# Kernel tuning notes

Measured on AMD Instinct MI355X. Metric: run time of the kernel, lower is better.

The kernel has to match this reference:

```python
import jax, jax.numpy as jnp
import numpy as np
import math

B, CIN, COUT, K, SD, H, W = 16, 512, 512, 3, 512, 32, 32


def setup_inputs() -> dict:
    key = jax.random.key(0)
    ks = jax.random.split(key, 7)
    return {
        "x": jax.random.normal(ks[0], (B, CIN, H, W), jnp.float32),
        "style": jax.random.normal(ks[1], (B, SD), jnp.float32),
        "noise": jax.random.normal(ks[2], (B, 1, H, W), jnp.float32),
        "weight": jax.random.normal(ks[3], (COUT, CIN, K, K), jnp.float32),
        "mod_w": jax.random.normal(ks[4], (CIN, SD), jnp.float32),
        "mod_b": jnp.ones((CIN,), jnp.float32),
        "noise_weight": jax.random.normal(ks[5], (1,), jnp.float32) * 0.1,
        "act_bias": jax.random.normal(ks[6], (COUT,), jnp.float32) * 0.1,
    }


def reference(x, style, noise, weight, mod_w, mod_b, noise_weight, act_bias):
    conv_scale = 1.0 / math.sqrt(CIN * K * K)  # equalized-lr scale of ModulatedConv2d
    mod_scale = 1.0 / math.sqrt(SD)            # EqualLinear scale (lr_mul=1)

    # style modulation: EqualLinear(style_dim -> in_channel), bias init 1
    s = style @ (mod_w.T * mod_scale) + mod_b              # [B, CIN]

    # per-sample modulated weights [B, COUT, CIN, K, K]
    w = conv_scale * weight[None] * s[:, None, :, None, None]

    # demodulation
    demod = jax.lax.rsqrt(jnp.sum(w * w, axis=(2, 3, 4)) + 1e-8)  # [B, COUT]
    w = w * demod[:, :, None, None, None]

    # grouped (per-sample) conv: vmap a single-sample conv over the batch
    pad = K // 2

    def conv1(xi, wi):
        return jax.lax.conv_general_dilated(
            xi[None], wi, window_strides=(1, 1),
            padding=[(pad, pad), (pad, pad)],
            dimension_numbers=("NCHW", "OIHW", "NCHW"))[0]

    out = jax.vmap(conv1)(x, w)  # [B, COUT, H, W]

    # NoiseInjection: out + weight * noise (scalar learned weight)
    out = out + noise_weight[0] * noise

    # FusedLeakyReLU: leaky_relu(out + bias, 0.2) * sqrt(2)
    out = jax.nn.leaky_relu(out + act_bias[None, :, None, None], 0.2) * math.sqrt(2.0)
    return out
```

## Files before the change

kernel.cpp:

```cpp
#include <hip/hip_runtime.h>
#include <cstdint>
#include <cstddef>

typedef unsigned short u16;
typedef __attribute__((ext_vector_type(8))) short short8;
typedef __attribute__((ext_vector_type(4))) float f32x4;

#define CIN   512
#define COUT  512
#define BATCH 16
#define HWSZ  1024
#define PADW  34

static constexpr float MOD_SCALE  = 0.044194173824159216f;
static constexpr float CONV_SCALE = 0.014731391274719739f;

#define WS_S    0
#define WS_DSC  (32*1024)
#define WS_WSQ  (64*1024)
#define WS_WBT  (64*1024 + 1024*1024)
#define WS_XSP  (WS_WBT + 9*512*512*2)

__device__ __forceinline__ u16 f2bf(float f) {
  union { float f; uint32_t u; } v; v.f = f;
  uint32_t r = v.u + 0x7fffu + ((v.u >> 16) & 1u);
  return (u16)(r >> 16);
}

__device__ __forceinline__ void gload16(const void* g, void* l) {
  __builtin_amdgcn_global_load_lds(
      (const __attribute__((address_space(1))) void*)g,
      (__attribute__((address_space(3))) void*)l, 16, 0, 0);
}

__global__ void k_style(const float* __restrict__ style, const float* __restrict__ mod_w,
                        const float* __restrict__ mod_b, float* __restrict__ s_out) {
  int gid  = blockIdx.x * blockDim.x + threadIdx.x;
  int w    = gid >> 6, lane = gid & 63;
  int b    = w >> 9, i = w & 511;
  const float4* st = (const float4*)(style + (size_t)b * 512);
  const float4* mw = (const float4*)(mod_w + (size_t)i * 512);
  float4 a0 = st[lane * 2], a1 = st[lane * 2 + 1];
  float4 w0 = mw[lane * 2], w1 = mw[lane * 2 + 1];
  float acc = a0.x*w0.x + a0.y*w0.y + a0.z*w0.z + a0.w*w0.w
            + a1.x*w1.x + a1.y*w1.y + a1.z*w1.z + a1.w*w1.w;
  #pragma unroll
  for (int off = 32; off; off >>= 1) acc += __shfl_xor(acc, off);
  if (lane == 0) s_out[w] = acc * MOD_SCALE + mod_b[i];
}

__global__ void k_wprep(const float* __restrict__ w, float* __restrict__ wsq,
                        u16* __restrict__ wbt2) {
  int idx = blockIdx.x * 256 + threadIdx.x;
  int o = idx >> 9, i = idx & 511;
  const float* p = w + (size_t)idx * 9;
  float a = 0.f;
  #pragma unroll
  for (int kxy = 0; kxy < 9; ++kxy) {
    float v = p[kxy];
    a += v * v;
    wbt2[((size_t)(kxy * 64 + (i >> 3)) * 512 + o) * 8 + (i & 7)] = f2bf(v);
  }
  wsq[idx] = a;
}

__global__ void k_dscale(const float* __restrict__ wsq, const float* __restrict__ s,
                         float* __restrict__ dsc) {
  int gid  = blockIdx.x * blockDim.x + threadIdx.x;
  int w    = gid >> 6, lane = gid & 63;
  int b    = w >> 9, o = w & 511;
  const float4* q4 = (const float4*)(wsq + (size_t)o * 512);
  const float4* s4 = (const float4*)(s   + (size_t)b * 512);
  float4 q0 = q4[lane * 2], q1 = q4[lane * 2 + 1];
  float4 t0 = s4[lane * 2], t1 = s4[lane * 2 + 1];
  float acc = q0.x*t0.x*t0.x + q0.y*t0.y*t0.y + q0.z*t0.z*t0.z + q0.w*t0.w*t0.w
            + q1.x*t1.x*t1.x + q1.y*t1.y*t1.y + q1.z*t1.z*t1.z + q1.w*t1.w*t1.w;
  #pragma unroll
  for (int off = 32; off; off >>= 1) acc += __shfl_xor(acc, off);
  if (lane == 0)
    dsc[w] = CONV_SCALE * rsqrtf(acc * CONV_SCALE * CONV_SCALE + 1e-8f);
}

__global__ void k_halo(u16* __restrict__ xsp) {
  int cell = blockIdx.x;
  int b = blockIdx.y;
  int y, x;
  if (cell < 34)       { y = 0;          x = cell; }
  else if (cell < 68)  { y = 33;         x = cell - 34; }
  else if (cell < 100) { y = cell - 67;  x = 0; }
  else                 { y = cell - 99;  x = 33; }
  uint32_t* p = (uint32_t*)(xsp + ((size_t)(b * PADW + y) * PADW + x) * 512);
  p[threadIdx.x] = 0;
}

__global__ void k_xs(const float* __restrict__ x, const float* __restrict__ s,
                     u16* __restrict__ xsp) {
  __shared__ float tile[64][33];
  int icb = blockIdx.x, y = blockIdx.y, b = blockIdx.z;
  int t = threadIdx.x;
  int i0 = icb * 64;
  int c  = t & 31;
  int r0 = t >> 5;
  #pragma unroll
  for (int it = 0; it < 8; ++it) {
    int row = r0 + it * 8;
    float sv = s[b * 512 + i0 + row];
    tile[row][c] = x[((size_t)(b * 512 + i0 + row)) * 1024 + y * 32 + c] * sv;
  }
  __syncthreads();
  int il = t & 63;
  int x0 = t >> 6;
  #pragma unroll
  for (int it = 0; it < 8; ++it) {
    int xc = x0 + it * 4;
    xsp[((size_t)((b * PADW + y + 1) * PADW) + (xc + 1)) * 512 + i0 + il] = f2bf(tile[il][xc]);
  }
}

__global__ __launch_bounds__(512, 2) void k_conv(
    const u16* __restrict__ wbt2, const u16* __restrict__ xsp,
    const float* __restrict__ dsc, const float* __restrict__ noise,
    const float* __restrict__ nw, const float* __restrict__ abias,
    float* __restrict__ out)
{
  __shared__ u16 Bld[3 * 8192];

  const int tid  = threadIdx.x;
  const int wave = tid >> 6, lane = tid & 63;

  const int bid = blockIdx.x;
  const int swz = (bid & 7) * 32 + (bid >> 3);
  const int o0 = (swz >> 7) << 8;
  const int m0 = (swz & 127) << 7;
  const int b  = m0 >> 10;

  const int wo = (wave >> 1) * 64;
  const int wm = (wave & 1) * 64;
  const int lrow = lane & 15;
  const int lk   = (lane >> 4) * 8;
  const int rsw  = (lrow & 7) << 3;

  const u16* pA = wbt2 + (size_t)(lane >> 4) * 4096 + (size_t)(o0 + wo + lrow) * 8;

  const int cc = (((lane & 7) ^ (lane >> 3)) * 8);
  const u16* gB[2]; int lBo[2];
  #pragma unroll
  for (int q = 0; q < 2; ++q) {
    int r = wave * 16 + q * 8 + (lane >> 3);
    int mg = m0 + r;
    int yy = (mg >> 5) & 31, xx = mg & 31;
    gB[q] = xsp + ((size_t)(b * PADW + yy) * PADW + xx) * 512 + cc;
    lBo[q] = (wave * 16 + q * 8) * 64;
  }

  f32x4 acc[4][4];
  #pragma unroll
  for (int i = 0; i < 4; ++i)
    #pragma unroll
    for (int j = 0; j < 4; ++j) acc[i][j] = (f32x4){0.f, 0.f, 0.f, 0.f};

  short8 av0[2][4], av1[2][4];

  auto avload = [&](int ks, short8 (&dst)[2][4]) {
    const u16* base = pA + (size_t)(ks >> 3) * 262144 + (size_t)(ks & 7) * 32768;
    #pragma unroll
    for (int kh = 0; kh < 2; ++kh)
      #pragma unroll
      for (int mi = 0; mi < 4; ++mi)
        dst[kh][mi] = *(const short8*)(base + kh * 16384 + mi * 128);
  };

  auto stageB = [&](int ks, int bufi) {
    int kxy = ks >> 3, ib = (ks & 7) << 6;
    int ky = kxy / 3, kx = kxy - ky * 3;
    int offB = ((ky * PADW + kx) << 9) + ib;
    int sb = bufi * 8192;
    #pragma unroll
    for (int q = 0; q < 2; ++q) gload16(gB[q] + offB, &Bld[sb + lBo[q]]);
  };

  auto compute = [&](const short8 (&av)[2][4], int bufi) {
    const int cb = bufi * 8192;
    __builtin_amdgcn_s_setprio(1);
    #pragma unroll
    for (int kh = 0; kh < 2; ++kh) {
      int kos = (kh * 32 + lk) ^ rsw;
      short8 bv[4];
      #pragma unroll
      for (int ni = 0; ni < 4; ++ni)
        bv[ni] = *(const short8*)&Bld[cb + (wm + ni * 16 + lrow) * 64 + kos];
      #pragma unroll
      for (int mi = 0; mi < 4; ++mi)
        #pragma unroll
        for (int ni = 0; ni < 4; ++ni)
          acc[mi][ni] = __builtin_amdgcn_mfma_f32_16x16x32_bf16(
              av[kh][mi], bv[ni], acc[mi][ni], 0, 0, 0);
    }
    __builtin_amdgcn_s_setprio(0);
  };

  stageB(0, 0);
  stageB(1, 1);
  avload(0, av0);

#define STEP(KS, AVCUR, AVNXT, BBUF, BNXT, DOAV, DOSTAGE, WN)            \
  {                                                                      \
    if (DOAV) avload((KS) + 1, AVNXT);                                   \
    __builtin_amdgcn_sched_barrier(0);                                   \
    asm volatile("s_waitcnt vmcnt(" #WN ")" ::: "memory");               \
    __builtin_amdgcn_s_barrier();                                        \
    __builtin_amdgcn_sched_barrier(0);                                   \
    if (DOSTAGE) stageB((KS) + 2, BNXT);                                 \
    compute(AVCUR, BBUF);                                                \
  }

  for (int t = 0; t < 11; ++t) {
    const int k0 = t * 6;
    STEP(k0 + 0, av0, av1, 0, 2, 1, 1, 8);
    STEP(k0 + 1, av1, av0, 1, 0, 1, 1, 8);
    STEP(k0 + 2, av0, av1, 2, 1, 1, 1, 8);
    STEP(k0 + 3, av1, av0, 0, 2, 1, 1, 8);
    STEP(k0 + 4, av0, av1, 1, 0, 1, 1, 8);
    STEP(k0 + 5, av1, av0, 2, 1, 1, 1, 8);
  }
  STEP(66, av0, av1, 0, 2, 1, 1, 8);
  STEP(67, av1, av0, 1, 0, 1, 1, 8);
  STEP(68, av0, av1, 2, 1, 1, 1, 8);
  STEP(69, av1, av0, 0, 2, 1, 1, 8);
  STEP(70, av0, av1, 1, 0, 1, 0, 8);
  STEP(71, av1, av0, 2, 1, 0, 0, 0);
#undef STEP

  const float nwv = nw[0];
  const int mrow = (lane >> 4) << 2;
  #pragma unroll
  for (int mi = 0; mi < 4; ++mi) {
    #pragma unroll
    for (int ni = 0; ni < 4; ++ni) {
      int mg = m0 + wm + ni * 16 + lrow;
      int hw = mg & 1023;
      float nz = nwv * noise[b * 1024 + hw];
      #pragma unroll
      for (int r = 0; r < 4; ++r) {
        int og = o0 + wo + mi * 16 + mrow + r;
        float v = acc[mi][ni][r] * dsc[b * 512 + og] + nz + abias[og];
        v = (v > 0.f ? v : 0.2f * v) * 1.4142135623730951f;
        out[(size_t)(b * 512 + og) * 1024 + hw] = v;
      }
    }
  }
}

extern "C" void kernel_launch(void* const* d_in, const int* in_sizes, int n_in,
                              void* d_out, int out_size, void* d_ws, size_t ws_size,
                              hipStream_t stream) {
  const float* x      = (const float*)d_in[0];
  const float* style  = (const float*)d_in[1];
  const float* noise  = (const float*)d_in[2];
  const float* weight = (const float*)d_in[3];
  const float* mod_w  = (const float*)d_in[4];
  const float* mod_b  = (const float*)d_in[5];
  const float* nw     = (const float*)d_in[6];
  const float* abias  = (const float*)d_in[7];
  float* out = (float*)d_out;

  char* ws = (char*)d_ws;
  float* s_buf = (float*)(ws + WS_S);
  float* dsc   = (float*)(ws + WS_DSC);
  float* wsq   = (float*)(ws + WS_WSQ);
  u16*   wbt2  = (u16*)(ws + WS_WBT);
  u16*   xsp   = (u16*)(ws + WS_XSP);

  k_halo  <<<dim3(132, 16), 256, 0, stream>>>(xsp);
  k_style <<<2048, 256, 0, stream>>>(style, mod_w, mod_b, s_buf);
  k_wprep <<<1024, 256, 0, stream>>>(weight, wsq, wbt2);
  k_dscale<<<2048, 256, 0, stream>>>(wsq, s_buf, dsc);
  k_xs    <<<dim3(8, 32, 16), 256, 0, stream>>>(x, s_buf, xsp);
  k_conv  <<<256, 512, 0, stream>>>(wbt2, xsp, dsc, noise, nw, abias, out);
}
```

Measured before the change: 105.2 us.

## Deepen conv B-tile pipeline to four LDS stages with register-prefetched fragments

```diff
diff --git a/kernel.cpp b/kernel.cpp
--- a/kernel.cpp
+++ b/kernel.cpp
@@ -123,7 +123,7 @@
     const float* __restrict__ nw, const float* __restrict__ abias,
     float* __restrict__ out)
 {
-  __shared__ u16 Bld[3 * 8192];
+  __shared__ u16 Bld[4 * 8192];
 
   const int tid  = threadIdx.x;
   const int wave = tid >> 6, lane = tid & 63;
@@ -160,6 +160,7 @@
     for (int j = 0; j < 4; ++j) acc[i][j] = (f32x4){0.f, 0.f, 0.f, 0.f};
 
   short8 av0[2][4], av1[2][4];
+  short8 bv0[2][4], bv1[2][4];
 
   auto avload = [&](int ks, short8 (&dst)[2][4]) {
     const u16* base = pA + (size_t)(ks >> 3) * 262144 + (size_t)(ks & 7) * 32768;
@@ -179,56 +180,61 @@
     for (int q = 0; q < 2; ++q) gload16(gB[q] + offB, &Bld[sb + lBo[q]]);
   };
 
-  auto compute = [&](const short8 (&av)[2][4], int bufi) {
+  auto bvread = [&](int bufi, short8 (&dst)[2][4]) {
     const int cb = bufi * 8192;
-    __builtin_amdgcn_s_setprio(1);
     #pragma unroll
     for (int kh = 0; kh < 2; ++kh) {
       int kos = (kh * 32 + lk) ^ rsw;
-      short8 bv[4];
       #pragma unroll
       for (int ni = 0; ni < 4; ++ni)
-        bv[ni] = *(const short8*)&Bld[cb + (wm + ni * 16 + lrow) * 64 + kos];
+        dst[kh][ni] = *(const short8*)&Bld[cb + (wm + ni * 16 + lrow) * 64 + kos];
+    }
+  };
+
+  auto compute = [&](const short8 (&av)[2][4], const short8 (&bv)[2][4]) {
+    __builtin_amdgcn_s_setprio(1);
+    #pragma unroll
+    for (int kh = 0; kh < 2; ++kh)
       #pragma unroll
       for (int mi = 0; mi < 4; ++mi)
         #pragma unroll
         for (int ni = 0; ni < 4; ++ni)
           acc[mi][ni] = __builtin_amdgcn_mfma_f32_16x16x32_bf16(
-              av[kh][mi], bv[ni], acc[mi][ni], 0, 0, 0);
-    }
+              av[kh][mi], bv[kh][ni], acc[mi][ni], 0, 0, 0);
     __builtin_amdgcn_s_setprio(0);
   };
 
   stageB(0, 0);
   stageB(1, 1);
+  stageB(2, 2);
   avload(0, av0);
-
-#define STEP(KS, AVCUR, AVNXT, BBUF, BNXT, DOAV, DOSTAGE, WN)            \
+  asm volatile("s_waitcnt vmcnt(12)" ::: "memory");
+  __builtin_amdgcn_s_barrier();
+  __builtin_amdgcn_sched_barrier(0);
+  bvread(0, bv0);
+
+#define STEP(KS, BSTG, BRD, AVC, AVN, BVC, BVN, DOSTG, DOAV, DOBV)       \
   {                                                                      \
-    if (DOAV) avload((KS) + 1, AVNXT);                                   \
-    __builtin_amdgcn_sched_barrier(0);                                   \
-    asm volatile("s_waitcnt vmcnt(" #WN ")" ::: "memory");               \
+    asm volatile("s_waitcnt vmcnt(10)" ::: "memory");                    \
     __builtin_amdgcn_s_barrier();                                        \
     __builtin_amdgcn_sched_barrier(0);                                   \
-    if (DOSTAGE) stageB((KS) + 2, BNXT);                                 \
-    compute(AVCUR, BBUF);                                                \
-  }
-
-  for (int t = 0; t < 11; ++t) {
-    const int k0 = t * 6;
-    STEP(k0 + 0, av0, av1, 0, 2, 1, 1, 8);
-    STEP(k0 + 1, av1, av0, 1, 0, 1, 1, 8);
-    STEP(k0 + 2, av0, av1, 2, 1, 1, 1, 8);
-    STEP(k0 + 3, av1, av0, 0, 2, 1, 1, 8);
-    STEP(k0 + 4, av0, av1, 1, 0, 1, 1, 8);
-    STEP(k0 + 5, av1, av0, 2, 1, 1, 1, 8);
-  }
-  STEP(66, av0, av1, 0, 2, 1, 1, 8);
-  STEP(67, av1, av0, 1, 0, 1, 1, 8);
-  STEP(68, av0, av1, 2, 1, 1, 1, 8);
-  STEP(69, av1, av0, 0, 2, 1, 1, 8);
-  STEP(70, av0, av1, 1, 0, 1, 0, 8);
-  STEP(71, av1, av0, 2, 1, 0, 0, 0);
+    if (DOSTG) stageB((KS) + 3, BSTG);                                   \
+    if (DOAV)  avload((KS) + 1, AVN);                                    \
+    if (DOBV)  bvread(BRD, BVN);                                         \
+    compute(AVC, BVC);                                                   \
+  }
+
+  for (int t = 0; t < 17; ++t) {
+    const int k0 = t * 4;
+    STEP(k0 + 0, 3, 1, av0, av1, bv0, bv1, 1, 1, 1);
+    STEP(k0 + 1, 0, 2, av1, av0, bv1, bv0, 1, 1, 1);
+    STEP(k0 + 2, 1, 3, av0, av1, bv0, bv1, 1, 1, 1);
+    STEP(k0 + 3, 2, 0, av1, av0, bv1, bv0, 1, 1, 1);
+  }
+  STEP(68, 3, 1, av0, av1, bv0, bv1, 1, 1, 1);
+  STEP(69, 0, 2, av1, av0, bv1, bv0, 0, 1, 1);
+  STEP(70, 1, 3, av0, av1, bv0, bv1, 0, 1, 1);
+  STEP(71, 2, 0, av1, av0, bv1, bv0, 0, 0, 0);
 #undef STEP
 
   const float nwv = nw[0];
```

New measurement: 109.4 us. 4.0% more time.

## Restructure conv GEMM to per-wave private LDS pipelines with larger warp tiles

Applied to the files above, without the earlier changes.

```diff
diff --git a/kernel.cpp b/kernel.cpp
--- a/kernel.cpp
+++ b/kernel.cpp
@@ -117,13 +117,13 @@
   }
 }
 
-__global__ __launch_bounds__(512, 2) void k_conv(
+__global__ __launch_bounds__(256, 1) void k_conv(
     const u16* __restrict__ wbt2, const u16* __restrict__ xsp,
     const float* __restrict__ dsc, const float* __restrict__ noise,
     const float* __restrict__ nw, const float* __restrict__ abias,
     float* __restrict__ out)
 {
-  __shared__ u16 Bld[3 * 8192];
+  extern __shared__ u16 SM[];
 
   const int tid  = threadIdx.x;
   const int wave = tid >> 6, lane = tid & 63;
@@ -134,107 +134,108 @@
   const int m0 = (swz & 127) << 7;
   const int b  = m0 >> 10;
 
-  const int wo = (wave >> 1) * 64;
-  const int wm = (wave & 1) * 64;
+  const int wo = (wave >> 1) << 7;
+  const int wm = (wave & 1) << 6;
   const int lrow = lane & 15;
-  const int lk   = (lane >> 4) * 8;
-  const int rsw  = (lrow & 7) << 3;
-
-  const u16* pA = wbt2 + (size_t)(lane >> 4) * 4096 + (size_t)(o0 + wo + lrow) * 8;
-
-  const int cc = (((lane & 7) ^ (lane >> 3)) * 8);
-  const u16* gB[2]; int lBo[2];
-  #pragma unroll
-  for (int q = 0; q < 2; ++q) {
-    int r = wave * 16 + q * 8 + (lane >> 3);
-    int mg = m0 + r;
+  const int kc   = lane >> 4;
+
+  u16* Abuf = &SM[wave * 18432];
+  u16* Bbuf = &SM[wave * 18432 + 12288];
+
+  const u16* gA = wbt2 + ((size_t)(o0 + wo) + lane) * 8;
+
+  const u16* gB[4];
+  #pragma unroll
+  for (int r = 0; r < 4; ++r) {
+    int row = r * 16 + (lane >> 2);
+    int ck  = (lane & 3) ^ ((row & 3) ^ ((row >> 2) & 3));
+    int mg  = m0 + wm + row;
     int yy = (mg >> 5) & 31, xx = mg & 31;
-    gB[q] = xsp + ((size_t)(b * PADW + yy) * PADW + xx) * 512 + cc;
-    lBo[q] = (wave * 16 + q * 8) * 64;
-  }
-
-  f32x4 acc[4][4];
-  #pragma unroll
-  for (int i = 0; i < 4; ++i)
+    gB[r] = xsp + ((size_t)(b * PADW + yy) * PADW + xx) * 512 + ck * 8;
+  }
+
+  f32x4 acc[8][4];
+  #pragma unroll
+  for (int i = 0; i < 8; ++i)
     #pragma unroll
     for (int j = 0; j < 4; ++j) acc[i][j] = (f32x4){0.f, 0.f, 0.f, 0.f};
 
-  short8 av0[2][4], av1[2][4];
-
-  auto avload = [&](int ks, short8 (&dst)[2][4]) {
-    const u16* base = pA + (size_t)(ks >> 3) * 262144 + (size_t)(ks & 7) * 32768;
-    #pragma unroll
-    for (int kh = 0; kh < 2; ++kh)
-      #pragma unroll
-      for (int mi = 0; mi < 4; ++mi)
-        dst[kh][mi] = *(const short8*)(base + kh * 16384 + mi * 128);
+  short8 av0[8], av1[8], bv0[4], bv1[4];
+
+  auto stage = [&](int ks, int s) {
+    const u16* as = gA + (size_t)(4 * ks) * 4096;
+    u16* ad = Abuf + s * 4096;
+    #pragma unroll
+    for (int r = 0; r < 8; ++r)
+      gload16(as + (r >> 1) * 4096 + (r & 1) * 512,
+              ad + (r >> 1) * 1024 + (r & 1) * 512);
+    int kxy = ks >> 4;
+    int ky = kxy / 3, kx = kxy - ky * 3;
+    int offB = ((ky * PADW + kx) << 9) + (ks & 15) * 32;
+    u16* bd = Bbuf + s * 2048;
+    #pragma unroll
+    for (int r = 0; r < 4; ++r)
+      gload16(gB[r] + offB, bd + r * 512);
   };
 
-  auto stageB = [&](int ks, int bufi) {
-    int kxy = ks >> 3, ib = (ks & 7) << 6;
-    int ky = kxy / 3, kx = kxy - ky * 3;
-    int offB = ((ky * PADW + kx) << 9) + ib;
-    int sb = bufi * 8192;
-    #pragma unroll
-    for (int q = 0; q < 2; ++q) gload16(gB[q] + offB, &Bld[sb + lBo[q]]);
-  };
-
-  auto compute = [&](const short8 (&av)[2][4], int bufi) {
-    const int cb = bufi * 8192;
-    __builtin_amdgcn_s_setprio(1);
-    #pragma unroll
-    for (int kh = 0; kh < 2; ++kh) {
-      int kos = (kh * 32 + lk) ^ rsw;
-      short8 bv[4];
-      #pragma unroll
-      for (int ni = 0; ni < 4; ++ni)
-        bv[ni] = *(const short8*)&Bld[cb + (wm + ni * 16 + lrow) * 64 + kos];
-      #pragma unroll
-      for (int mi = 0; mi < 4; ++mi)
-        #pragma unroll
-        for (int ni = 0; ni < 4; ++ni)
-          acc[mi][ni] = __builtin_amdgcn_mfma_f32_16x16x32_bf16(
-              av[kh][mi], bv[ni], acc[mi][ni], 0, 0, 0);
-    }
-    __builtin_amdgcn_s_setprio(0);
-  };
-
-  stageB(0, 0);
-  stageB(1, 1);
-  avload(0, av0);
-
-#define STEP(KS, AVCUR, AVNXT, BBUF, BNXT, DOAV, DOSTAGE, WN)            \
+#define RD(S, AV, BV)                                                     \
+  {                                                                       \
+    const u16* pa = Abuf + (S) * 4096 + kc * 1024 + lrow * 8;             \
+    _Pragma("unroll")                                                     \
+    for (int mi = 0; mi < 8; ++mi)                                        \
+      AV[mi] = *(const short8*)(pa + mi * 128);                           \
+    _Pragma("unroll")                                                     \
+    for (int ni = 0; ni < 4; ++ni) {                                      \
+      int row = ni * 16 + lrow;                                           \
+      int ckr = kc ^ ((row & 3) ^ ((row >> 2) & 3));                      \
+      BV[ni] = *(const short8*)(Bbuf + (S) * 2048 + row * 32 + ckr * 8);  \
+    }                                                                     \
+  }
+
+#define COMPUTE(AV, BV)                                                   \
+  _Pragma("unroll")                                                       \
+  for (int mi = 0; mi < 8; ++mi)                                          \
+    _Pragma("unroll")                                                     \
+    for (int ni = 0; ni < 4; ++ni)                                        \
+      acc[mi][ni] = __builtin_amdgcn_mfma_f32_16x16x32_bf16(              \
+          AV[mi], BV[ni], acc[mi][ni], 0, 0, 0);
+
+  stage(0, 0);
+  stage(1, 1);
+  asm volatile("s_waitcnt vmcnt(12)" ::: "memory");
+  RD(0, av0, bv0);
+
+#define STEP(KS, SNX, SRD, AVN, BVN, AVC, BVC, DOSTG, DORD, VM)          \
   {                                                                      \
-    if (DOAV) avload((KS) + 1, AVNXT);                                   \
-    __builtin_amdgcn_sched_barrier(0);                                   \
-    asm volatile("s_waitcnt vmcnt(" #WN ")" ::: "memory");               \
-    __builtin_amdgcn_s_barrier();                                        \
-    __builtin_amdgcn_sched_barrier(0);                                   \
-    if (DOSTAGE) stageB((KS) + 2, BNXT);                                 \
-    compute(AVCUR, BBUF);                                                \
-  }
-
-  for (int t = 0; t < 11; ++t) {
+    if (DOSTG) stage((KS) + 2, SNX);                                     \
+    asm volatile("s_waitcnt vmcnt(" #VM ")" ::: "memory");               \
+    if (DORD) RD(SRD, AVN, BVN);                                         \
+    COMPUTE(AVC, BVC);                                                   \
+  }
+
+  for (int t = 0; t < 23; ++t) {
     const int k0 = t * 6;
-    STEP(k0 + 0, av0, av1, 0, 2, 1, 1, 8);
-    STEP(k0 + 1, av1, av0, 1, 0, 1, 1, 8);
-    STEP(k0 + 2, av0, av1, 2, 1, 1, 1, 8);
-    STEP(k0 + 3, av1, av0, 0, 2, 1, 1, 8);
-    STEP(k0 + 4, av0, av1, 1, 0, 1, 1, 8);
-    STEP(k0 + 5, av1, av0, 2, 1, 1, 1, 8);
-  }
-  STEP(66, av0, av1, 0, 2, 1, 1, 8);
-  STEP(67, av1, av0, 1, 0, 1, 1, 8);
-  STEP(68, av0, av1, 2, 1, 1, 1, 8);
-  STEP(69, av1, av0, 0, 2, 1, 1, 8);
-  STEP(70, av0, av1, 1, 0, 1, 0, 8);
-  STEP(71, av1, av0, 2, 1, 0, 0, 0);
+    STEP(k0 + 0, 2, 1, av1, bv1, av0, bv0, 1, 1, 12);
+    STEP(k0 + 1, 0, 2, av0, bv0, av1, bv1, 1, 1, 12);
+    STEP(k0 + 2, 1, 0, av1, bv1, av0, bv0, 1, 1, 12);
+    STEP(k0 + 3, 2, 1, av0, bv0, av1, bv1, 1, 1, 12);
+    STEP(k0 + 4, 0, 2, av1, bv1, av0, bv0, 1, 1, 12);
+    STEP(k0 + 5, 1, 0, av0, bv0, av1, bv1, 1, 1, 12);
+  }
+  STEP(138, 2, 1, av1, bv1, av0, bv0, 1, 1, 12);
+  STEP(139, 0, 2, av0, bv0, av1, bv1, 1, 1, 12);
+  STEP(140, 1, 0, av1, bv1, av0, bv0, 1, 1, 12);
+  STEP(141, 2, 1, av0, bv0, av1, bv1, 1, 1, 12);
+  STEP(142, 0, 2, av1, bv1, av0, bv0, 0, 1, 0);
+  STEP(143, 0, 0, av0, bv0, av1, bv1, 0, 0, 0);
 #undef STEP
+#undef RD
+#undef COMPUTE
 
   const float nwv = nw[0];
   const int mrow = (lane >> 4) << 2;
   #pragma unroll
-  for (int mi = 0; mi < 4; ++mi) {
+  for (int mi = 0; mi < 8; ++mi) {
     #pragma unroll
     for (int ni = 0; ni < 4; ++ni) {
       int mg = m0 + wm + ni * 16 + lrow;
@@ -271,10 +272,13 @@
   u16*   wbt2  = (u16*)(ws + WS_WBT);
   u16*   xsp   = (u16*)(ws + WS_XSP);
 
+  hipFuncSetAttribute((const void*)k_conv,
+                      hipFuncAttributeMaxDynamicSharedMemorySize, 147456);
+
   k_halo  <<<dim3(132, 16), 256, 0, stream>>>(xsp);
   k_style <<<2048, 256, 0, stream>>>(style, mod_w, mod_b, s_buf);
   k_wprep <<<1024, 256, 0, stream>>>(weight, wsq, wbt2);
   k_dscale<<<2048, 256, 0, stream>>>(wsq, s_buf, dsc);
   k_xs    <<<dim3(8, 32, 16), 256, 0, stream>>>(x, s_buf, xsp);
-  k_conv  <<<256, 512, 0, stream>>>(wbt2, xsp, dsc, noise, nw, abias, out);
-}
+  k_conv  <<<256, 256, 147456, stream>>>(wbt2, xsp, dsc, noise, nw, abias, out);
+}
```

New measurement: 116.0 us. +10.3%, slower.

## Stage input halo tile once per channel chunk and reuse across all 3x3 taps

Applied to the files above, without the earlier changes.

```diff
diff --git a/kernel.cpp b/kernel.cpp
--- a/kernel.cpp
+++ b/kernel.cpp
@@ -25,12 +25,6 @@
   union { float f; uint32_t u; } v; v.f = f;
   uint32_t r = v.u + 0x7fffu + ((v.u >> 16) & 1u);
   return (u16)(r >> 16);
-}
-
-__device__ __forceinline__ void gload16(const void* g, void* l) {
-  __builtin_amdgcn_global_load_lds(
-      (const __attribute__((address_space(1))) void*)g,
-      (__attribute__((address_space(3))) void*)l, 16, 0, 0);
 }
 
 __global__ void k_style(const float* __restrict__ style, const float* __restrict__ mod_w,
@@ -117,13 +111,13 @@
   }
 }
 
-__global__ __launch_bounds__(512, 2) void k_conv(
+__global__ __launch_bounds__(512, 1) void k_conv(
     const u16* __restrict__ wbt2, const u16* __restrict__ xsp,
     const float* __restrict__ dsc, const float* __restrict__ noise,
     const float* __restrict__ nw, const float* __restrict__ abias,
     float* __restrict__ out)
 {
-  __shared__ u16 Bld[3 * 8192];
+  __shared__ u16 H[2][13824];
 
   const int tid  = threadIdx.x;
   const int wave = tid >> 6, lane = tid & 63;
@@ -133,24 +127,42 @@
   const int o0 = (swz >> 7) << 8;
   const int m0 = (swz & 127) << 7;
   const int b  = m0 >> 10;
+  const int y0 = (m0 & 1023) >> 5;
 
   const int wo = (wave >> 1) * 64;
   const int wm = (wave & 1) * 64;
   const int lrow = lane & 15;
-  const int lk   = (lane >> 4) * 8;
-  const int rsw  = (lrow & 7) << 3;
-
-  const u16* pA = wbt2 + (size_t)(lane >> 4) * 4096 + (size_t)(o0 + wo + lrow) * 8;
-
-  const int cc = (((lane & 7) ^ (lane >> 3)) * 8);
-  const u16* gB[2]; int lBo[2];
-  #pragma unroll
-  for (int q = 0; q < 2; ++q) {
-    int r = wave * 16 + q * 8 + (lane >> 3);
-    int mg = m0 + r;
-    int yy = (mg >> 5) & 31, xx = mg & 31;
-    gB[q] = xsp + ((size_t)(b * PADW + yy) * PADW + xx) * 512 + cc;
-    lBo[q] = (wave * 16 + q * 8) * 64;
+  const int g    = lane >> 4;
+
+  const u16* pA = wbt2 + (size_t)g * 4096 + (size_t)(o0 + wo + lrow) * 8;
+
+  int offs[4][3][2];
+  #pragma unroll
+  for (int ni = 0; ni < 4; ++ni) {
+    int mloc = wm + ni * 16 + lrow;
+    int yb = mloc >> 5, xb = mloc & 31;
+    #pragma unroll
+    for (int kx = 0; kx < 3; ++kx) {
+      int xx = xb + kx;
+      #pragma unroll
+      for (int kh = 0; kh < 2; ++kh) {
+        int c = (kh * 4 + g) ^ (xx & 7);
+        offs[ni][kx][kh] = (((yb * 36 + xx) * 64) + c * 8) * 2;
+      }
+    }
+  }
+
+  int hsrc[4], hdst[4];
+  bool hval[4];
+  #pragma unroll
+  for (int r = 0; r < 4; ++r) {
+    int T = r * 512 + wave * 64 + lane;
+    hval[r] = (T < 1632);
+    int Tc = hval[r] ? T : 0;
+    int yy = Tc / 272, rem = Tc % 272;
+    int xx = rem >> 3, c = rem & 7;
+    hsrc[r] = ((b * 34 + y0 + yy) * 34 + xx) * 512 + c * 8;
+    hdst[r] = (yy * 36 + xx) * 64 + ((c ^ (xx & 7)) * 8);
   }
 
   f32x4 acc[4][4];
@@ -160,76 +172,91 @@
     for (int j = 0; j < 4; ++j) acc[i][j] = (f32x4){0.f, 0.f, 0.f, 0.f};
 
   short8 av0[2][4], av1[2][4];
-
-  auto avload = [&](int ks, short8 (&dst)[2][4]) {
-    const u16* base = pA + (size_t)(ks >> 3) * 262144 + (size_t)(ks & 7) * 32768;
-    #pragma unroll
-    for (int kh = 0; kh < 2; ++kh)
-      #pragma unroll
-      for (int mi = 0; mi < 4; ++mi)
-        dst[kh][mi] = *(const short8*)(base + kh * 16384 + mi * 128);
-  };
-
-  auto stageB = [&](int ks, int bufi) {
-    int kxy = ks >> 3, ib = (ks & 7) << 6;
-    int ky = kxy / 3, kx = kxy - ky * 3;
-    int offB = ((ky * PADW + kx) << 9) + ib;
-    int sb = bufi * 8192;
-    #pragma unroll
-    for (int q = 0; q < 2; ++q) gload16(gB[q] + offB, &Bld[sb + lBo[q]]);
-  };
-
-  auto compute = [&](const short8 (&av)[2][4], int bufi) {
-    const int cb = bufi * 8192;
-    __builtin_amdgcn_s_setprio(1);
-    #pragma unroll
-    for (int kh = 0; kh < 2; ++kh) {
-      int kos = (kh * 32 + lk) ^ rsw;
-      short8 bv[4];
-      #pragma unroll
-      for (int ni = 0; ni < 4; ++ni)
-        bv[ni] = *(const short8*)&Bld[cb + (wm + ni * 16 + lrow) * 64 + kos];
-      #pragma unroll
-      for (int mi = 0; mi < 4; ++mi)
-        #pragma unroll
-        for (int ni = 0; ni < 4; ++ni)
-          acc[mi][ni] = __builtin_amdgcn_mfma_f32_16x16x32_bf16(
-              av[kh][mi], bv[ni], acc[mi][ni], 0, 0, 0);
-    }
-    __builtin_amdgcn_s_setprio(0);
-  };
-
-  stageB(0, 0);
-  stageB(1, 1);
-  avload(0, av0);
-
-#define STEP(KS, AVCUR, AVNXT, BBUF, BNXT, DOAV, DOSTAGE, WN)            \
-  {                                                                      \
-    if (DOAV) avload((KS) + 1, AVNXT);                                   \
-    __builtin_amdgcn_sched_barrier(0);                                   \
-    asm volatile("s_waitcnt vmcnt(" #WN ")" ::: "memory");               \
-    __builtin_amdgcn_s_barrier();                                        \
-    __builtin_amdgcn_sched_barrier(0);                                   \
-    if (DOSTAGE) stageB((KS) + 2, BNXT);                                 \
-    compute(AVCUR, BBUF);                                                \
-  }
-
-  for (int t = 0; t < 11; ++t) {
-    const int k0 = t * 6;
-    STEP(k0 + 0, av0, av1, 0, 2, 1, 1, 8);
-    STEP(k0 + 1, av1, av0, 1, 0, 1, 1, 8);
-    STEP(k0 + 2, av0, av1, 2, 1, 1, 1, 8);
-    STEP(k0 + 3, av1, av0, 0, 2, 1, 1, 8);
-    STEP(k0 + 4, av0, av1, 1, 0, 1, 1, 8);
-    STEP(k0 + 5, av1, av0, 2, 1, 1, 1, 8);
-  }
-  STEP(66, av0, av1, 0, 2, 1, 1, 8);
-  STEP(67, av1, av0, 1, 0, 1, 1, 8);
-  STEP(68, av0, av1, 2, 1, 1, 1, 8);
-  STEP(69, av1, av0, 0, 2, 1, 1, 8);
-  STEP(70, av0, av1, 1, 0, 1, 0, 8);
-  STEP(71, av1, av0, 2, 1, 0, 0, 0);
-#undef STEP
+  short8 hv[4];
+
+#define AVLOAD(NP, NK, DST)                                               \
+  { const u16* ab = pA + (NK) * 262144 + (NP) * 32768;                    \
+    _Pragma("unroll")                                                     \
+    for (int kh = 0; kh < 2; ++kh)                                        \
+      _Pragma("unroll")                                                   \
+      for (int mi = 0; mi < 4; ++mi)                                      \
+        DST[kh][mi] = *(const short8*)(ab + kh * 16384 + mi * 128); }
+
+#define TILE(PP, KXY, AVC, AVN, HC, HN, DOLD, DOH0, DOH4)                 \
+  {                                                                       \
+    if (DOH0) {                                                           \
+      _Pragma("unroll")                                                   \
+      for (int r = 0; r < 4; ++r)                                         \
+        if (hval[r])                                                      \
+          hv[r] = *(const short8*)(xsp + hsrc[r] + ((PP) + 1) * 64);      \
+    }                                                                     \
+    if (DOH4) {                                                           \
+      _Pragma("unroll")                                                   \
+      for (int r = 0; r < 4; ++r)                                         \
+        if (hval[r]) *(short8*)&H[HN][hdst[r]] = hv[r];                   \
+    }                                                                     \
+    if (DOLD) {                                                           \
+      const int NP = ((KXY) < 8) ? (PP) : (PP) + 1;                       \
+      const int NK = ((KXY) < 8) ? (KXY) + 1 : 0;                         \
+      AVLOAD(NP, NK, AVN);                                                \
+    }                                                                     \
+    {                                                                     \
+      const int ky = (KXY) / 3, kx = (KXY) % 3;                           \
+      const char* hb = (const char*)&H[HC][0] + ky * 4608;                \
+      short8 bv[4];                                                       \
+      _Pragma("unroll")                                                   \
+      for (int ni = 0; ni < 4; ++ni)                                      \
+        bv[ni] = *(const short8*)(hb + offs[ni][kx][0]);                  \
+      _Pragma("unroll")                                                   \
+      for (int mi = 0; mi < 4; ++mi)                                      \
+        _Pragma("unroll")                                                 \
+        for (int ni = 0; ni < 4; ++ni)                                    \
+          acc[mi][ni] = __builtin_amdgcn_mfma_f32_16x16x32_bf16(          \
+              AVC[0][mi], bv[ni], acc[mi][ni], 0, 0, 0);                  \
+      _Pragma("unroll")                                                   \
+      for (int ni = 0; ni < 4; ++ni)                                      \
+        bv[ni] = *(const short8*)(hb + offs[ni][kx][1]);                  \
+      _Pragma("unroll")                                                   \
+      for (int mi = 0; mi < 4; ++mi)                                      \
+        _Pragma("unroll")                                                 \
+        for (int ni = 0; ni < 4; ++ni)                                    \
+          acc[mi][ni] = __builtin_amdgcn_mfma_f32_16x16x32_bf16(          \
+              AVC[1][mi], bv[ni], acc[mi][ni], 0, 0, 0);                  \
+    }                                                                     \
+  }
+
+#define PASS(PP, HC, HN, A, B, DOSTG, DOLDLAST)                           \
+  TILE(PP, 0, A, B, HC, HN, 1, DOSTG, 0)                                  \
+  TILE(PP, 1, B, A, HC, HN, 1, 0, 0)                                      \
+  TILE(PP, 2, A, B, HC, HN, 1, 0, 0)                                      \
+  TILE(PP, 3, B, A, HC, HN, 1, 0, 0)                                      \
+  TILE(PP, 4, A, B, HC, HN, 1, 0, DOSTG)                                  \
+  TILE(PP, 5, B, A, HC, HN, 1, 0, 0)                                      \
+  TILE(PP, 6, A, B, HC, HN, 1, 0, 0)                                      \
+  TILE(PP, 7, B, A, HC, HN, 1, 0, 0)                                      \
+  TILE(PP, 8, A, B, HC, HN, DOLDLAST, 0, 0)                               \
+  asm volatile("s_waitcnt lgkmcnt(0)" ::: "memory");                      \
+  __builtin_amdgcn_s_barrier();
+
+  #pragma unroll
+  for (int r = 0; r < 4; ++r)
+    if (hval[r]) hv[r] = *(const short8*)(xsp + hsrc[r]);
+  #pragma unroll
+  for (int r = 0; r < 4; ++r)
+    if (hval[r]) *(short8*)&H[0][hdst[r]] = hv[r];
+  AVLOAD(0, 0, av0);
+  asm volatile("s_waitcnt lgkmcnt(0)" ::: "memory");
+  __builtin_amdgcn_s_barrier();
+
+  for (int pp = 0; pp < 6; pp += 2) {
+    PASS(pp,     0, 1, av0, av1, 1, 1)
+    PASS(pp + 1, 1, 0, av1, av0, 1, 1)
+  }
+  PASS(6, 0, 1, av0, av1, 1, 1)
+  PASS(7, 1, 0, av1, av0, 0, 0)
+#undef PASS
+#undef TILE
+#undef AVLOAD
 
   const float nwv = nw[0];
   const int mrow = (lane >> 4) << 2;
```

Measured after the change: 117.0 us. +11.2%, slower.
